# Kernel optimization log

Measured on AMD Instinct MI355X. Metric: run time of the kernel, lower is better.

Reference implementation:

```python
import jax, jax.numpy as jnp
import numpy as np

N = 8192
IN_CH = 256
OUT_CH = 256


def setup_inputs() -> dict:
    key = jax.random.key(0)
    k1, k2, k3, k4, k5 = jax.random.split(key, 5)
    features = jax.random.normal(k1, (N, IN_CH), dtype=jnp.float32)
    wavelets = jax.random.normal(k2, (N, N), dtype=jnp.float32)
    wavelets_inv = jax.random.normal(k3, (N, N), dtype=jnp.float32)
    # parameters
    # xavier uniform for weight_matrix
    limit = np.sqrt(6.0 / (IN_CH + OUT_CH)).astype(np.float32)
    weight_matrix = jax.random.uniform(k4, (IN_CH, OUT_CH), minval=-limit, maxval=limit, dtype=jnp.float32)
    filt = jax.random.uniform(k5, (N,), minval=0.9, maxval=1.1, dtype=jnp.float32)
    return {"features": features, "wavelets": wavelets, "wavelets_inv": wavelets_inv,
            "weight_matrix": weight_matrix, "filt": filt}


def reference(features, wavelets, wavelets_inv, weight_matrix, filt):
    # transformed = features @ W                    [N, out]
    transformed = features @ weight_matrix
    # spectral = wavelets_inv @ transformed         [N, out]
    spectral = wavelets_inv @ transformed
    # torch.diag(filter) @ spectral == filt[:, None] * spectral (avoid NxN diag GEMM)
    filtered = filt[:, None] * spectral
    # output = wavelets @ filtered                  [N, out]
    return wavelets @ filtered
```

## Files before the change

### kernel.cpp

```cpp
#include <hip/hip_runtime.h>
#include <hip/hip_bf16.h>
#include <stdint.h>
#include <stddef.h>

typedef __bf16 bf16;
typedef float f32x4 __attribute__((ext_vector_type(4)));
typedef bf16 bf16x8 __attribute__((ext_vector_type(8)));
typedef bf16 bf16x4 __attribute__((ext_vector_type(4)));

#define MROWS 8192
#define NOUT 256
#define BM 32
#define BK 128
#define NTHREADS 512

#define LDS_A_BYTES (BM * BK * 2)

#define SCHED0 __builtin_amdgcn_sched_barrier(0)
#define SBAR __builtin_amdgcn_s_barrier()


template <bool SCALE, bool OUTT>
__global__ __launch_bounds__(NTHREADS, 1) void gemm_deep(
    const float* __restrict__ A, const bf16* __restrict__ Bp,
    const float* __restrict__ filt, void* __restrict__ outp,
    const int K, const int lda) {
  __shared__ char lds[4][LDS_A_BYTES];
  const int t = threadIdx.x;
  const int w = t >> 6;
  const int l = t & 63;
  const int m0 = blockIdx.x * BM;
  const int NT = K / BK;

  const int ar = t >> 4;
  const int acb = t & 15;
  const float* gA = A + (size_t)(m0 + ar) * (size_t)lda + acb * 8;
  const int a_lds_off = (ar * (BK * 2) + acb * 16) ^ ((ar & 7) << 4);

  int aoff[2][4];
#pragma unroll
  for (int af = 0; af < 2; ++af)
#pragma unroll
    for (int ak = 0; ak < 4; ++ak) {
      const int r = af * 16 + (l & 15);
      const int kb = ak * 64 + (l >> 4) * 16;
      aoff[af][ak] = (r * (BK * 2) + kb) ^ ((r & 7) << 4);
    }

  const char* pBw = (const char*)Bp + w * 8192 + l * 16;

  f32x4 acc[2][2] = {};

  f32x4 A0a = __builtin_nontemporal_load((const f32x4*)gA);
  f32x4 A0b = __builtin_nontemporal_load((const f32x4*)gA + 1);
  f32x4 A1a = __builtin_nontemporal_load((const f32x4*)(gA + BK));
  f32x4 A1b = __builtin_nontemporal_load((const f32x4*)(gA + BK) + 1);
  bf16x8 B0[2][4], B1[2][4];
#pragma unroll
  for (int bfi = 0; bfi < 2; ++bfi)
#pragma unroll
    for (int ak = 0; ak < 4; ++ak)
      B0[bfi][ak] = *(const bf16x8*)(pBw + (bfi * 4 + ak) * 1024);
  f32x4 g0a = __builtin_nontemporal_load((const f32x4*)(gA + 2 * BK));
  f32x4 g0b = __builtin_nontemporal_load((const f32x4*)(gA + 2 * BK) + 1);
  f32x4 g1a, g1b;
  {
    bf16x8 pk;
#pragma unroll
    for (int j = 0; j < 4; ++j) { pk[j] = (bf16)A0a[j]; pk[j + 4] = (bf16)A0b[j]; }
    *(bf16x8*)(lds[0] + a_lds_off) = pk;
#pragma unroll
    for (int j = 0; j < 4; ++j) { pk[j] = (bf16)A1a[j]; pk[j + 4] = (bf16)A1b[j]; }
    *(bf16x8*)(lds[1] + a_lds_off) = pk;
  }
  asm volatile("s_waitcnt lgkmcnt(0)" ::: "memory");
  SBAR;
  SCHED0;
  bf16x8 f0[2][4], f1[2][4];
#pragma unroll
  for (int af = 0; af < 2; ++af)
#pragma unroll
    for (int ak = 0; ak < 4; ++ak)
      f0[af][ak] = *(const bf16x8*)(lds[0] + aoff[af][ak]);
  SCHED0;

#define BODY_D(TS, SW, SR, FC, FN, BCr, BNr, AC0, AC1, AN0, AN1)              \
  {                                                                           \
    const size_t kb1 = (size_t)((((TS) + 1) < NT ? ((TS) + 1) : 0)) << 16;    \
    _Pragma("unroll") for (int bfi = 0; bfi < 2; ++bfi)                       \
        _Pragma("unroll") for (int ak = 0; ak < 4; ++ak)                      \
            BNr[bfi][ak] =                                                    \
                *(const bf16x8*)(pBw + kb1 + (bfi * 4 + ak) * 1024);          \
    SCHED0;                                                                   \
    const int ka3 = ((((TS) + 3) < NT) ? ((TS) + 3) : 0) * BK;                \
    AN0 = __builtin_nontemporal_load((const f32x4*)(gA + ka3));               \
    AN1 = __builtin_nontemporal_load((const f32x4*)(gA + ka3) + 1);           \
    SCHED0;                                                                   \
    {                                                                         \
      bf16x8 pk;                                                              \
      _Pragma("unroll") for (int j = 0; j < 4; ++j) {                         \
        pk[j] = (bf16)AC0[j];                                                 \
        pk[j + 4] = (bf16)AC1[j];                                             \
      }                                                                       \
      *(bf16x8*)(lds[SW] + a_lds_off) = pk;                                   \
    }                                                                         \
    SCHED0;                                                                   \
    _Pragma("unroll") for (int af = 0; af < 2; ++af)                          \
        _Pragma("unroll") for (int ak = 0; ak < 4; ++ak)                      \
            FN[af][ak] = *(const bf16x8*)(lds[SR] + aoff[af][ak]);            \
    SCHED0;                                                                   \
    __builtin_amdgcn_s_setprio(1);                                            \
    _Pragma("unroll") for (int ak = 0; ak < 4; ++ak)                          \
        _Pragma("unroll") for (int af = 0; af < 2; ++af)                      \
            _Pragma("unroll") for (int bfi = 0; bfi < 2; ++bfi)               \
                acc[af][bfi] = __builtin_amdgcn_mfma_f32_16x16x32_bf16(       \
                    FC[af][ak], BCr[bfi][ak], acc[af][bfi], 0, 0, 0);         \
    __builtin_amdgcn_s_setprio(0);                                            \
    SCHED0;                                                                   \
    asm volatile("s_waitcnt lgkmcnt(0)" ::: "memory");                        \
    SBAR;                                                                     \
    SCHED0;                                                                   \
  }

  for (int ts = 0; ts < NT; ts += 4) {
    BODY_D(ts, 2, 1, f0, f1, B0, B1, g0a, g0b, g1a, g1b);
    BODY_D(ts + 1, 3, 2, f1, f0, B1, B0, g1a, g1b, g0a, g0b);
    BODY_D(ts + 2, 0, 3, f0, f1, B0, B1, g0a, g0b, g1a, g1b);
    BODY_D(ts + 3, 1, 0, f1, f0, B1, B0, g1a, g1b, g0a, g0b);
  }
#undef BODY_D

#pragma unroll
  for (int af = 0; af < 2; ++af)
#pragma unroll
    for (int bfi = 0; bfi < 2; ++bfi) {
      const int mb = m0 + af * 16 + (l >> 4) * 4;
      const int n = w * 32 + bfi * 16 + (l & 15);
      f32x4 v = acc[af][bfi];
      if (SCALE) {
#pragma unroll
        for (int j = 0; j < 4; ++j) v[j] *= filt[mb + j];
      }
      if (OUTT) {
        bf16x4 pv;
#pragma unroll
        for (int j = 0; j < 4; ++j) pv[j] = (bf16)v[j];
        const int tsq = mb >> 7, wq = n >> 5, bq = (n >> 4) & 1, aq = (mb >> 5) & 3;
        const int lq = ((mb >> 3) & 3) * 16 + (n & 15);
        char* dst = (char*)outp +
                    (size_t)(((tsq * 64 + wq * 8 + bq * 4 + aq) << 10) + lq * 16 +
                             (mb & 7) * 2);
        *(bf16x4*)dst = pv;
      } else {
        float* po = (float*)outp + (size_t)mb * NOUT + n;
#pragma unroll
        for (int j = 0; j < 4; ++j) po[(size_t)j * NOUT] = v[j];
      }
    }
}

template <bool SCALE, bool OUTT>
__global__ __launch_bounds__(NTHREADS, 1) void gemm_small(
    const float* __restrict__ A, const bf16* __restrict__ Bp,
    const float* __restrict__ filt, void* __restrict__ outp,
    const int K, const int lda) {
  __shared__ char lds[2][LDS_A_BYTES];
  const int t = threadIdx.x;
  const int w = t >> 6;
  const int l = t & 63;
  const int m0 = blockIdx.x * BM;
  const int NT = K / BK;

  const int ar = t >> 4;
  const int acb = t & 15;
  const float* gA = A + (size_t)(m0 + ar) * (size_t)lda + acb * 8;
  const int a_lds_off = (ar * (BK * 2) + acb * 16) ^ ((ar & 7) << 4);

  int aoff[2][4];
#pragma unroll
  for (int af = 0; af < 2; ++af)
#pragma unroll
    for (int ak = 0; ak < 4; ++ak) {
      const int r = af * 16 + (l & 15);
      const int kb = ak * 64 + (l >> 4) * 16;
      aoff[af][ak] = (r * (BK * 2) + kb) ^ ((r & 7) << 4);
    }

  const char* pBw = (const char*)Bp + w * 8192 + l * 16;

  f32x4 acc[2][2] = {};

  f32x4 aS0a = __builtin_nontemporal_load((const f32x4*)gA);
  f32x4 aS0b = __builtin_nontemporal_load((const f32x4*)gA + 1);
  f32x4 aS1a = __builtin_nontemporal_load((const f32x4*)(gA + BK));
  f32x4 aS1b = __builtin_nontemporal_load((const f32x4*)(gA + BK) + 1);
  bf16x8 Bc[2][4], Bn[2][4];
#pragma unroll
  for (int bfi = 0; bfi < 2; ++bfi)
#pragma unroll
    for (int ak = 0; ak < 4; ++ak)
      Bc[bfi][ak] = *(const bf16x8*)(pBw + (bfi * 4 + ak) * 1024);
  {
    bf16x8 pk;
#pragma unroll
    for (int j = 0; j < 4; ++j) { pk[j] = (bf16)aS0a[j]; pk[j + 4] = (bf16)aS0b[j]; }
    *(bf16x8*)(lds[0] + a_lds_off) = pk;
  }
  asm volatile("s_waitcnt lgkmcnt(0)" ::: "memory");
  SBAR;
  SCHED0;

#define BODY_S(TS, P, BCUR, BNXT, AW0, AW1, AL0, AL1)                         \
  {                                                                           \
    const char* bb = lds[P];                                                  \
    bf16x8 afr[2][4];                                                         \
    _Pragma("unroll") for (int af = 0; af < 2; ++af)                          \
        _Pragma("unroll") for (int ak = 0; ak < 4; ++ak)                      \
            afr[af][ak] = *(const bf16x8*)(bb + aoff[af][ak]);                \
    SCHED0;                                                                   \
    const size_t kb1 = (size_t)((((TS) + 1) < NT ? ((TS) + 1) : 0)) << 16;    \
    _Pragma("unroll") for (int bfi = 0; bfi < 2; ++bfi)                       \
        _Pragma("unroll") for (int ak = 0; ak < 4; ++ak)                      \
            BNXT[bfi][ak] =                                                   \
                *(const bf16x8*)(pBw + kb1 + (bfi * 4 + ak) * 1024);          \
    SCHED0;                                                                   \
    const int ka2 = (((TS) + 2) < NT ? ((TS) + 2) : 0) * BK;                  \
    AL0 = __builtin_nontemporal_load((const f32x4*)(gA + ka2));               \
    AL1 = __builtin_nontemporal_load((const f32x4*)(gA + ka2) + 1);           \
    SCHED0;                                                                   \
    asm volatile("s_waitcnt lgkmcnt(0)" ::: "memory");                        \
    SCHED0;                                                                   \
    __builtin_amdgcn_s_setprio(1);                                            \
    _Pragma("unroll") for (int ak = 0; ak < 4; ++ak)                          \
        _Pragma("unroll") for (int af = 0; af < 2; ++af)                      \
            _Pragma("unroll") for (int bfi = 0; bfi < 2; ++bfi)               \
                acc[af][bfi] = __builtin_amdgcn_mfma_f32_16x16x32_bf16(       \
                    afr[af][ak], BCUR[bfi][ak], acc[af][bfi], 0, 0, 0);       \
    __builtin_amdgcn_s_setprio(0);                                            \
    SCHED0;                                                                   \
    {                                                                         \
      bf16x8 pk;                                                              \
      _Pragma("unroll") for (int j = 0; j < 4; ++j) {                         \
        pk[j] = (bf16)AW0[j];                                                 \
        pk[j + 4] = (bf16)AW1[j];                                             \
      }                                                                       \
      *(bf16x8*)(lds[P ^ 1] + a_lds_off) = pk;                                \
    }                                                                         \
    asm volatile("s_waitcnt lgkmcnt(0)" ::: "memory");                        \
    SBAR;                                                                     \
    SCHED0;                                                                   \
  }

  for (int ts = 0; ts < NT; ts += 2) {
    BODY_S(ts, 0, Bc, Bn, aS1a, aS1b, aS0a, aS0b);
    BODY_S(ts + 1, 1, Bn, Bc, aS0a, aS0b, aS1a, aS1b);
  }
#undef BODY_S

#pragma unroll
  for (int af = 0; af < 2; ++af)
#pragma unroll
    for (int bfi = 0; bfi < 2; ++bfi) {
      const int mb = m0 + af * 16 + (l >> 4) * 4;
      const int n = w * 32 + bfi * 16 + (l & 15);
      f32x4 v = acc[af][bfi];
      if (SCALE) {
#pragma unroll
        for (int j = 0; j < 4; ++j) v[j] *= filt[mb + j];
      }
      if (OUTT) {
        bf16x4 pv;
#pragma unroll
        for (int j = 0; j < 4; ++j) pv[j] = (bf16)v[j];
        const int tsq = mb >> 7, wq = n >> 5, bq = (n >> 4) & 1, aq = (mb >> 5) & 3;
        const int lq = ((mb >> 3) & 3) * 16 + (n & 15);
        char* dst = (char*)outp +
                    (size_t)(((tsq * 64 + wq * 8 + bq * 4 + aq) << 10) + lq * 16 +
                             (mb & 7) * 2);
        *(bf16x4*)dst = pv;
      } else {
        float* po = (float*)outp + (size_t)mb * NOUT + n;
#pragma unroll
        for (int j = 0; j < 4; ++j) po[(size_t)j * NOUT] = v[j];
      }
    }
}

__global__ void prep_wt(const float* __restrict__ W, bf16* __restrict__ Wp) {
  const int k = blockIdx.x;
  const int n = threadIdx.x;
  const int off = (((k >> 7) * 64 + (n >> 5) * 8 + ((n >> 4) & 1) * 4 +
                    ((k >> 5) & 3)) << 10) +
                  (((k >> 3) & 3) * 16 + (n & 15)) * 16 + (k & 7) * 2;
  *(bf16*)((char*)Wp + off) = (bf16)W[k * 256 + n];
}

extern "C" void kernel_launch(void* const* d_in, const int* in_sizes, int n_in,
                              void* d_out, int out_size, void* d_ws, size_t ws_size,
                              hipStream_t stream) {
  const float* features = (const float*)d_in[0];
  const float* wavelets = (const float*)d_in[1];
  const float* wavelets_inv = (const float*)d_in[2];
  const float* W = (const float*)d_in[3];
  const float* filt = (const float*)d_in[4];
  float* out = (float*)d_out;

  char* ws = (char*)d_ws;
  bf16* Wp = (bf16*)ws;
  bf16* Tp = (bf16*)(ws + 131072);
  bf16* Fp = (bf16*)(ws + 131072 + 4194304);

  prep_wt<<<256, 256, 0, stream>>>(W, Wp);
  gemm_small<false, true><<<256, NTHREADS, 0, stream>>>(features, Wp, nullptr, Tp, 256, 256);
  gemm_deep<true, true><<<256, NTHREADS, 0, stream>>>(wavelets_inv, Tp, filt, Fp, 8192, 8192);
  gemm_deep<false, false><<<256, NTHREADS, 0, stream>>>(wavelets, Fp, nullptr, out, 8192, 8192);
}
```

Measured before the change: 194.3 us.

## Restructure deep GEMM pipeline into double-buffered 512-wide K phases

Replaces the four-slot per-128-K LDS ring with two 32x512 bf16 slots. Each slot is filled once per four K-steps, so the workgroup barrier runs once per phase instead of once per step. A-tile global loads for the next phase are issued during the first two steps and converted and stored to the other slot at the end of the phase. This cuts barrier and sync overhead in the memory-bound wavelet GEMMs, at the cost of more live registers (8 prefetch vectors) and a burstier write and load pattern.

Measured after the change: 184.2 us. -5.2%, faster.

```diff
diff --git a/kernel.cpp b/kernel.cpp
--- a/kernel.cpp
+++ b/kernel.cpp
@@ -12,123 +12,132 @@
 #define NOUT 256
 #define BM 32
 #define BK 128
+#define PSTEPS 4
+#define PK (BK * PSTEPS)
 #define NTHREADS 512
 
-#define LDS_A_BYTES (BM * BK * 2)
+#define SLOT_BYTES (BM * PK * 2)
+#define LDS_SMALL (BM * BK * 2)
 
 #define SCHED0 __builtin_amdgcn_sched_barrier(0)
 #define SBAR __builtin_amdgcn_s_barrier()
 
 
 template <bool SCALE, bool OUTT>
-__global__ __launch_bounds__(NTHREADS, 1) void gemm_deep(
+__global__ __launch_bounds__(NTHREADS, 1) void gemm_big(
     const float* __restrict__ A, const bf16* __restrict__ Bp,
     const float* __restrict__ filt, void* __restrict__ outp,
     const int K, const int lda) {
-  __shared__ char lds[4][LDS_A_BYTES];
+  __shared__ char lds[2][SLOT_BYTES];
   const int t = threadIdx.x;
   const int w = t >> 6;
   const int l = t & 63;
   const int m0 = blockIdx.x * BM;
   const int NT = K / BK;
+  const int NP = K / PK;
 
   const int ar = t >> 4;
-  const int acb = t & 15;
-  const float* gA = A + (size_t)(m0 + ar) * (size_t)lda + acb * 8;
-  const int a_lds_off = (ar * (BK * 2) + acb * 16) ^ ((ar & 7) << 4);
-
-  int aoff[2][4];
+  const int ac = t & 15;
+  const float* gA = A + (size_t)(m0 + ar) * (size_t)lda + ac * 8;
+
+  int awoff[4];
+#pragma unroll
+  for (int j = 0; j < 4; ++j)
+    awoff[j] = ar * 2048 / 2 + ((j * 256 + ac * 16) ^ ((ar & 7) << 4));
+
+  int aoff0[2][4];
 #pragma unroll
   for (int af = 0; af < 2; ++af)
 #pragma unroll
     for (int ak = 0; ak < 4; ++ak) {
       const int r = af * 16 + (l & 15);
-      const int kb = ak * 64 + (l >> 4) * 16;
-      aoff[af][ak] = (r * (BK * 2) + kb) ^ ((r & 7) << 4);
+      aoff0[af][ak] = r * 1024 + ((ak * 64 + (l >> 4) * 16) ^ ((r & 7) << 4));
     }
 
   const char* pBw = (const char*)Bp + w * 8192 + l * 16;
 
   f32x4 acc[2][2] = {};
-
-  f32x4 A0a = __builtin_nontemporal_load((const f32x4*)gA);
-  f32x4 A0b = __builtin_nontemporal_load((const f32x4*)gA + 1);
-  f32x4 A1a = __builtin_nontemporal_load((const f32x4*)(gA + BK));
-  f32x4 A1b = __builtin_nontemporal_load((const f32x4*)(gA + BK) + 1);
-  bf16x8 B0[2][4], B1[2][4];
+  f32x4 pA[8];
+  bf16x8 Breg[2][2][4];
+
+#pragma unroll
+  for (int q = 0; q < 8; ++q)
+    pA[q] = __builtin_nontemporal_load(
+        (const f32x4*)(gA + (q >> 1) * 128 + (q & 1) * 4));
 #pragma unroll
   for (int bfi = 0; bfi < 2; ++bfi)
 #pragma unroll
     for (int ak = 0; ak < 4; ++ak)
-      B0[bfi][ak] = *(const bf16x8*)(pBw + (bfi * 4 + ak) * 1024);
-  f32x4 g0a = __builtin_nontemporal_load((const f32x4*)(gA + 2 * BK));
-  f32x4 g0b = __builtin_nontemporal_load((const f32x4*)(gA + 2 * BK) + 1);
-  f32x4 g1a, g1b;
-  {
+      Breg[0][bfi][ak] = *(const bf16x8*)(pBw + (bfi * 4 + ak) * 1024);
+#pragma unroll
+  for (int j = 0; j < 4; ++j) {
     bf16x8 pk;
 #pragma unroll
-    for (int j = 0; j < 4; ++j) { pk[j] = (bf16)A0a[j]; pk[j + 4] = (bf16)A0b[j]; }
-    *(bf16x8*)(lds[0] + a_lds_off) = pk;
-#pragma unroll
-    for (int j = 0; j < 4; ++j) { pk[j] = (bf16)A1a[j]; pk[j + 4] = (bf16)A1b[j]; }
-    *(bf16x8*)(lds[1] + a_lds_off) = pk;
+    for (int e = 0; e < 4; ++e) {
+      pk[e] = (bf16)pA[2 * j][e];
+      pk[e + 4] = (bf16)pA[2 * j + 1][e];
+    }
+    *(bf16x8*)(lds[0] + awoff[j]) = pk;
   }
   asm volatile("s_waitcnt lgkmcnt(0)" ::: "memory");
   SBAR;
-  SCHED0;
-  bf16x8 f0[2][4], f1[2][4];
-#pragma unroll
-  for (int af = 0; af < 2; ++af)
-#pragma unroll
-    for (int ak = 0; ak < 4; ++ak)
-      f0[af][ak] = *(const bf16x8*)(lds[0] + aoff[af][ak]);
-  SCHED0;
-
-#define BODY_D(TS, SW, SR, FC, FN, BCr, BNr, AC0, AC1, AN0, AN1)              \
-  {                                                                           \
-    const size_t kb1 = (size_t)((((TS) + 1) < NT ? ((TS) + 1) : 0)) << 16;    \
-    _Pragma("unroll") for (int bfi = 0; bfi < 2; ++bfi)                       \
-        _Pragma("unroll") for (int ak = 0; ak < 4; ++ak)                      \
-            BNr[bfi][ak] =                                                    \
-                *(const bf16x8*)(pBw + kb1 + (bfi * 4 + ak) * 1024);          \
-    SCHED0;                                                                   \
-    const int ka3 = ((((TS) + 3) < NT) ? ((TS) + 3) : 0) * BK;                \
-    AN0 = __builtin_nontemporal_load((const f32x4*)(gA + ka3));               \
-    AN1 = __builtin_nontemporal_load((const f32x4*)(gA + ka3) + 1);           \
-    SCHED0;                                                                   \
-    {                                                                         \
-      bf16x8 pk;                                                              \
-      _Pragma("unroll") for (int j = 0; j < 4; ++j) {                         \
-        pk[j] = (bf16)AC0[j];                                                 \
-        pk[j + 4] = (bf16)AC1[j];                                             \
-      }                                                                       \
-      *(bf16x8*)(lds[SW] + a_lds_off) = pk;                                   \
-    }                                                                         \
-    SCHED0;                                                                   \
-    _Pragma("unroll") for (int af = 0; af < 2; ++af)                          \
-        _Pragma("unroll") for (int ak = 0; ak < 4; ++ak)                      \
-            FN[af][ak] = *(const bf16x8*)(lds[SR] + aoff[af][ak]);            \
-    SCHED0;                                                                   \
-    __builtin_amdgcn_s_setprio(1);                                            \
-    _Pragma("unroll") for (int ak = 0; ak < 4; ++ak)                          \
-        _Pragma("unroll") for (int af = 0; af < 2; ++af)                      \
-            _Pragma("unroll") for (int bfi = 0; bfi < 2; ++bfi)               \
-                acc[af][bfi] = __builtin_amdgcn_mfma_f32_16x16x32_bf16(       \
-                    FC[af][ak], BCr[bfi][ak], acc[af][bfi], 0, 0, 0);         \
-    __builtin_amdgcn_s_setprio(0);                                            \
-    SCHED0;                                                                   \
-    asm volatile("s_waitcnt lgkmcnt(0)" ::: "memory");                        \
-    SBAR;                                                                     \
-    SCHED0;                                                                   \
-  }
-
-  for (int ts = 0; ts < NT; ts += 4) {
-    BODY_D(ts, 2, 1, f0, f1, B0, B1, g0a, g0b, g1a, g1b);
-    BODY_D(ts + 1, 3, 2, f1, f0, B1, B0, g1a, g1b, g0a, g0b);
-    BODY_D(ts + 2, 0, 3, f0, f1, B0, B1, g0a, g0b, g1a, g1b);
-    BODY_D(ts + 3, 1, 0, f1, f0, B1, B0, g1a, g1b, g0a, g0b);
-  }
-#undef BODY_D
+
+  for (int p = 0; p < NP; ++p) {
+    const int pn = (p + 1 < NP) ? p + 1 : 0;
+    const char* rslot = lds[p & 1];
+    char* wslot = lds[(p + 1) & 1];
+    const float* gApn = gA + (size_t)pn * PK;
+
+#pragma unroll
+    for (int s = 0; s < PSTEPS; ++s) {
+      const int ts = p * PSTEPS + s;
+      const size_t kb1 = (size_t)((ts + 1 < NT) ? ts + 1 : 0) << 16;
+#pragma unroll
+      for (int bfi = 0; bfi < 2; ++bfi)
+#pragma unroll
+        for (int ak = 0; ak < 4; ++ak)
+          Breg[(s + 1) & 1][bfi][ak] =
+              *(const bf16x8*)(pBw + kb1 + (bfi * 4 + ak) * 1024);
+      SCHED0;
+      if (s < 2) {
+#pragma unroll
+        for (int q4 = 0; q4 < 4; ++q4) {
+          const int q = s * 4 + q4;
+          pA[q] = __builtin_nontemporal_load(
+              (const f32x4*)(gApn + (q >> 1) * 128 + (q & 1) * 4));
+        }
+        SCHED0;
+      }
+      bf16x8 afr[2][4];
+#pragma unroll
+      for (int af = 0; af < 2; ++af)
+#pragma unroll
+        for (int ak = 0; ak < 4; ++ak)
+          afr[af][ak] = *(const bf16x8*)(rslot + aoff0[af][ak] + s * 256);
+      __builtin_amdgcn_s_setprio(1);
+#pragma unroll
+      for (int ak = 0; ak < 4; ++ak)
+#pragma unroll
+        for (int af = 0; af < 2; ++af)
+#pragma unroll
+          for (int bfi = 0; bfi < 2; ++bfi)
+            acc[af][bfi] = __builtin_amdgcn_mfma_f32_16x16x32_bf16(
+                afr[af][ak], Breg[s & 1][bfi][ak], acc[af][bfi], 0, 0, 0);
+      __builtin_amdgcn_s_setprio(0);
+    }
+#pragma unroll
+    for (int j = 0; j < 4; ++j) {
+      bf16x8 pk;
+#pragma unroll
+      for (int e = 0; e < 4; ++e) {
+        pk[e] = (bf16)pA[2 * j][e];
+        pk[e + 4] = (bf16)pA[2 * j + 1][e];
+      }
+      *(bf16x8*)(wslot + awoff[j]) = pk;
+    }
+    asm volatile("s_waitcnt lgkmcnt(0)" ::: "memory");
+    SBAR;
+  }
 
 #pragma unroll
   for (int af = 0; af < 2; ++af)
@@ -164,7 +173,7 @@
     const float* __restrict__ A, const bf16* __restrict__ Bp,
     const float* __restrict__ filt, void* __restrict__ outp,
     const int K, const int lda) {
-  __shared__ char lds[2][LDS_A_BYTES];
+  __shared__ char lds[2][LDS_SMALL];
   const int t = threadIdx.x;
   const int w = t >> 6;
   const int l = t & 63;
@@ -312,6 +321,6 @@
 
   prep_wt<<<256, 256, 0, stream>>>(W, Wp);
   gemm_small<false, true><<<256, NTHREADS, 0, stream>>>(features, Wp, nullptr, Tp, 256, 256);
-  gemm_deep<true, true><<<256, NTHREADS, 0, stream>>>(wavelets_inv, Tp, filt, Fp, 8192, 8192);
-  gemm_deep<false, false><<<256, NTHREADS, 0, stream>>>(wavelets, Fp, nullptr, out, 8192, 8192);
+  gemm_big<true, true><<<256, NTHREADS, 0, stream>>>(wavelets_inv, Tp, filt, Fp, 8192, 8192);
+  gemm_big<false, false><<<256, NTHREADS, 0, stream>>>(wavelets, Fp, nullptr, out, 8192, 8192);
 }
```
